# Optimization experiments

Measured on AMD Instinct MI355X. Metric: run time of the kernel, lower is better.

## Reference

```python
import jax, jax.numpy as jnp
import numpy as np

B, H, S, Dh = 4, 16, 2048, 64
NEG = -1.0e9


def setup_inputs() -> dict:
    key = jax.random.key(0)
    kq, kk, kv = jax.random.split(key, 3)
    q = jax.random.normal(kq, (B, H, S, Dh), dtype=jnp.float32)
    k = jax.random.normal(kk, (B, H, S, Dh), dtype=jnp.float32)
    v = jax.random.normal(kv, (B, H, S, Dh), dtype=jnp.float32)
    # causal mask: 1.0 where attention is disallowed (j > i), matching mask * -1e9
    mask = jnp.triu(jnp.ones((S, S), dtype=jnp.float32), k=1)[None, None, :, :]
    return {"q": q, "k": k, "v": v, "mask": mask}


def reference(q, k, v, mask):
    # scaled dot-product attention: softmax(QK^T / sqrt(Dh) + mask * -1e9) V
    dim_k = jnp.asarray(k.shape[-1], dtype=jnp.float32)
    logits = jnp.einsum("bhsd,bhtd->bhst", q, k) / jnp.sqrt(dim_k)
    logits = logits + mask * NEG
    weights = jax.nn.softmax(logits, axis=-1)
    return jnp.einsum("bhst,bhtd->bhsd", weights, v)
```

## Files before the change

kernel.cpp:

```cpp
#include <hip/hip_runtime.h>

#define S_LEN 2048
#define DH 64

typedef float f32x4 __attribute__((ext_vector_type(4)));
typedef __bf16 bf16x8 __attribute__((ext_vector_type(8)));

#define PTS 72
#define MFMA16(A, B, C) __builtin_amdgcn_mfma_f32_16x16x32_bf16(A, B, C, 0, 0, 0)

__device__ __forceinline__ unsigned short f2bf(float f) {
    unsigned u = __builtin_bit_cast(unsigned, f);
    u += 0x7fffu + ((u >> 16) & 1u);
    return (unsigned short)(u >> 16);
}

__device__ __forceinline__ uint4 pack8(const float* s) {
    unsigned short h[8];
#pragma unroll
    for (int i = 0; i < 8; ++i) h[i] = f2bf(s[i]);
    return *(const uint4*)h;
}

__device__ __forceinline__ unsigned pack_tr(float a, float b) {
    return __builtin_amdgcn_perm(__builtin_bit_cast(unsigned, b),
                                 __builtin_bit_cast(unsigned, a), 0x07060302u);
}

__device__ __forceinline__ bf16x8 ld128(const unsigned short* p) {
    return __builtin_bit_cast(bf16x8, *(const uint4*)p);
}

__device__ __forceinline__ bf16x8 ones8() {
    uint4 ou; ou.x = 0x3F803F80u; ou.y = ou.x; ou.z = ou.x; ou.w = ou.x;
    return __builtin_bit_cast(bf16x8, ou);
}

__global__ __launch_bounds__(256) void prep_kv(const float* __restrict__ k,
                                               const float* __restrict__ v,
                                               uint4* __restrict__ kimg,
                                               uint4* __restrict__ vimg) {
    __shared__ unsigned short tr[64 * 40];
    const int bid = blockIdx.x;
    const int t = threadIdx.x;
    if (bid < 4096) {
        const int r = t >> 3, b = t & 7;
        const int srcblk = b ^ (r & 7);
        const float* src = k + ((size_t)bid * 32 + r) * 64 + srcblk * 8;
        float buf[8];
        *(float4*)&buf[0] = *(const float4*)src;
        *(float4*)&buf[4] = *(const float4*)(src + 4);
        kimg[(size_t)bid * 256 + t] = pack8(buf);
    } else {
        const int vb = bid - 4096;
        const int r = t >> 3, cb = t & 7;
        const float* src = v + ((size_t)vb * 32 + r) * 64 + cb * 8;
        float buf[8];
        *(float4*)&buf[0] = *(const float4*)src;
        *(float4*)&buf[4] = *(const float4*)(src + 4);
#pragma unroll
        for (int i = 0; i < 8; ++i)
            tr[(cb * 8 + i) * 40 + r] = f2bf(buf[i]);
        __syncthreads();
        const int d = t >> 2, kb = t & 3;
        const int skb = kb ^ ((d >> 1) & 3);
        vimg[(size_t)vb * 256 + t] = *(const uint4*)&tr[d * 40 + skb * 8];
    }
}

template <int DIAG>
__device__ __forceinline__ void body64(
    const unsigned short* __restrict__ kt, const unsigned short* __restrict__ vt,
    unsigned short* __restrict__ pw0, unsigned short* __restrict__ pw1,
    const bf16x8* qf, f32x4 acc[2][4], f32x4* accl,
    int jt, int qbase, int quad, int c)
{
    const int sw = c & 7;
    const bf16x8 ones = ones8();
    const int MTN = (DIAG == 1) ? 2 : 4;

#pragma unroll
    for (int mt = 0; mt < MTN; ++mt) {
        const unsigned short* kr = kt + (mt * 16 + c) * 64;
        bf16x8 ka0 = ld128(kr + ((quad ^ sw) << 3));
        bf16x8 ka1 = ld128(kr + (((quad | 4) ^ sw) << 3));
        f32x4 s0 = (f32x4){0.f, 0.f, 0.f, 0.f};
        f32x4 s1 = (f32x4){0.f, 0.f, 0.f, 0.f};
        s0 = MFMA16(ka0, qf[0], s0);  s0 = MFMA16(ka1, qf[1], s0);
        s1 = MFMA16(ka0, qf[2], s1);  s1 = MFMA16(ka1, qf[3], s1);

        const bool MASKMT = (DIAG == 1) || (DIAG == 2 && mt >= 2);
#pragma unroll
        for (int s = 0; s < 2; ++s) {
            const f32x4 st = s ? s1 : s0;
            const int ig = qbase + s * 16 + c;
            float p[4];
#pragma unroll
            for (int r = 0; r < 4; ++r) {
                float e = __builtin_amdgcn_exp2f(st[r]);
                if (MASKMT) {
                    const int jg = jt * 64 + mt * 16 + quad * 4 + r;
                    e = (jg > ig) ? 0.f : e;
                }
                p[r] = e;
            }
            unsigned a = pack_tr(p[0], p[1]);
            unsigned b = pack_tr(p[2], p[3]);
            unsigned* pb = (unsigned*)(s ? pw1 : pw0) + c * (PTS / 2) + mt * 8 + quad * 2;
            *(uint2*)pb = make_uint2(a, b);
        }
    }

    bf16x8 pf00 = ld128(pw0 + c * PTS + quad * 8);
    bf16x8 pf10 = ld128(pw1 + c * PTS + quad * 8);
    accl[0] = MFMA16(pf00, ones, accl[0]);
    accl[1] = MFMA16(pf10, ones, accl[1]);
    bf16x8 pf01, pf11;
    if (DIAG != 1) {
        pf01 = ld128(pw0 + c * PTS + 32 + quad * 8);
        pf11 = ld128(pw1 + c * PTS + 32 + quad * 8);
        accl[0] = MFMA16(pf01, ones, accl[0]);
        accl[1] = MFMA16(pf11, ones, accl[1]);
    }

    const int vsw = (c >> 1) & 3;
#pragma unroll
    for (int dc = 0; dc < 4; ++dc) {
        const unsigned short* vr = vt + (dc * 16 + c) * 32 + ((quad ^ vsw) << 3);
        bf16x8 vf0 = ld128(vr);
        acc[0][dc] = MFMA16(pf00, vf0, acc[0][dc]);
        acc[1][dc] = MFMA16(pf10, vf0, acc[1][dc]);
        if (DIAG != 1) {
            bf16x8 vf1 = ld128(vr + 2048);
            acc[0][dc] = MFMA16(pf01, vf1, acc[0][dc]);
            acc[1][dc] = MFMA16(pf11, vf1, acc[1][dc]);
        }
    }
}

__global__ __launch_bounds__(256, 4) void fa_kernel(
    const float* __restrict__ q,
    const uint4* __restrict__ kimg,
    const uint4* __restrict__ vimg,
    float* __restrict__ out)
{
    __shared__ unsigned short kt[64 * 64];
    __shared__ unsigned short vt[2 * 64 * 32];
    __shared__ unsigned short pt[4][2][16 * PTS];

    const int tid  = threadIdx.x;
    const int lane = tid & 63;
    const int wave = tid >> 6;
    const int quad = lane >> 4;
    const int c    = lane & 15;

    const int bid = blockIdx.x;
    const int bh  = bid & 63;
    static const int qperm[16] = {15, 14, 13, 12, 8, 9, 10, 11,
                                  6, 5, 4, 3, 1, 2, 7, 0};
    const int qblk = qperm[bid >> 6];

    const int wt      = qblk * 4 + wave;
    const int qbase   = wt * 32;
    const int my_diag = wt >> 1;
    const int jt_last = 2 * qblk + 1;

    const size_t head_off = (size_t)bh * S_LEN * DH;

    const float SCALE = 0.125f * 1.4426950408889634f;
    bf16x8 qf[4];
#pragma unroll
    for (int s = 0; s < 2; ++s) {
        const float* qrow = q + head_off + (size_t)(qbase + s * 16 + c) * DH;
        float t0[8], t1[8];
#pragma unroll
        for (int i = 0; i < 8; ++i) t0[i] = qrow[quad * 8 + i] * SCALE;
#pragma unroll
        for (int i = 0; i < 8; ++i) t1[i] = qrow[32 + quad * 8 + i] * SCALE;
        qf[s * 2 + 0] = __builtin_bit_cast(bf16x8, pack8(t0));
        qf[s * 2 + 1] = __builtin_bit_cast(bf16x8, pack8(t1));
    }

    f32x4 acc[2][4];
#pragma unroll
    for (int s = 0; s < 2; ++s)
#pragma unroll
        for (int dc = 0; dc < 4; ++dc) acc[s][dc] = (f32x4){0.f, 0.f, 0.f, 0.f};
    f32x4 accl[2];
    accl[0] = (f32x4){0.f, 0.f, 0.f, 0.f};
    accl[1] = (f32x4){0.f, 0.f, 0.f, 0.f};

    const uint4* kin = kimg + (size_t)bh * 64 * 256 + tid;
    const uint4* vin = vimg + (size_t)bh * 64 * 256 + tid;
    unsigned short* pw0 = pt[wave][0];
    unsigned short* pw1 = pt[wave][1];

    uint4 kA = kin[0], kB = kin[256];
    uint4 vA = vin[0], vB = vin[256];
    for (int jt = 0; jt <= jt_last; ++jt) {
        __syncthreads();
        ((uint4*)kt)[tid] = kA;  ((uint4*)kt)[tid + 256] = kB;
        ((uint4*)vt)[tid] = vA;  ((uint4*)vt)[tid + 256] = vB;
        if (jt < jt_last) {
            kA = kin[(jt + 1) * 512];  kB = kin[(jt + 1) * 512 + 256];
            vA = vin[(jt + 1) * 512];  vB = vin[(jt + 1) * 512 + 256];
        }
        __syncthreads();

        if (jt < my_diag) {
            body64<0>(kt, vt, pw0, pw1, qf, acc, accl, jt, qbase, quad, c);
        } else if (jt == my_diag) {
            if ((wt & 1) == 0)
                body64<1>(kt, vt, pw0, pw1, qf, acc, accl, jt, qbase, quad, c);
            else
                body64<2>(kt, vt, pw0, pw1, qf, acc, accl, jt, qbase, quad, c);
        }
    }

    float* ob = out + head_off;
#pragma unroll
    for (int s = 0; s < 2; ++s) {
        float linv[4];
#pragma unroll
        for (int r = 0; r < 4; ++r) linv[r] = 1.0f / accl[s][r];
#pragma unroll
        for (int dc = 0; dc < 4; ++dc)
#pragma unroll
            for (int r = 0; r < 4; ++r) {
                const size_t idx =
                    (size_t)(qbase + s * 16 + quad * 4 + r) * DH + dc * 16 + c;
                ob[idx] = acc[s][dc][r] * linv[r];
            }
    }
}

#define KT_STRIDE 88
#define VT_STRIDE 36
__global__ __launch_bounds__(256) void fa_kernel_fb(
    const float* __restrict__ q, const float* __restrict__ k,
    const float* __restrict__ v, float* __restrict__ out)
{
    __shared__ unsigned short kts[32 * KT_STRIDE];
    __shared__ unsigned short vts[64 * VT_STRIDE];
    __shared__ unsigned short pts[4][16 * 40];
    const int tid = threadIdx.x, lane = tid & 63, wave = tid >> 6;
    const int quad = lane >> 4, c = lane & 15;
    const int bid = blockIdx.x, bh = bid & 63, qblk = 31 - (bid >> 6);
    const int qtile = qblk * 4 + wave, qbase = qtile * 16;
    const int my_diag = qtile >> 1, jt_last = (qblk * 4 + 3) >> 1;
    const size_t head_off = (size_t)bh * S_LEN * DH;
    const float* qrow = q + head_off + (size_t)(qbase + c) * DH;
    float qtmp[8];
#pragma unroll
    for (int i = 0; i < 8; ++i) qtmp[i] = qrow[quad * 8 + i];
    bf16x8 qf0 = __builtin_bit_cast(bf16x8, pack8(qtmp));
#pragma unroll
    for (int i = 0; i < 8; ++i) qtmp[i] = qrow[32 + quad * 8 + i];
    bf16x8 qf1 = __builtin_bit_cast(bf16x8, pack8(qtmp));
    f32x4 acc[4];
#pragma unroll
    for (int dc = 0; dc < 4; ++dc) acc[dc] = (f32x4){0.f, 0.f, 0.f, 0.f};
    float m_run = -1e30f, l_run = 0.f;
    const int ig = qbase + c;
    const int srow = tid >> 3, sdb = tid & 7;
    const int vcol = (((srow >> 3) ^ (sdb & 3)) << 3) | (srow & 7);
    const float LOG2E = 1.4426950408889634f;
    for (int jt = 0; jt <= jt_last; ++jt) {
        __syncthreads();
        {
            const size_t g = head_off + (size_t)(jt * 32 + srow) * DH + sdb * 8;
            float kbuf[8];
            *(float4*)&kbuf[0] = *(const float4*)(k + g);
            *(float4*)&kbuf[4] = *(const float4*)(k + g + 4);
            *(uint4*)&kts[srow * KT_STRIDE + sdb * 8] = pack8(kbuf);
            float vbuf[8];
            *(float4*)&vbuf[0] = *(const float4*)(v + g);
            *(float4*)&vbuf[4] = *(const float4*)(v + g + 4);
#pragma unroll
            for (int i = 0; i < 8; ++i)
                vts[(sdb * 8 + i) * VT_STRIDE + vcol] = f2bf(vbuf[i]);
        }
        __syncthreads();
        if (jt > my_diag) continue;
        f32x4 st[2];
#pragma unroll
        for (int mt = 0; mt < 2; ++mt) {
            const unsigned short* krow = &kts[(mt * 16 + c) * KT_STRIDE + quad * 8];
            bf16x8 ka0 = __builtin_bit_cast(bf16x8, *(const uint4*)krow);
            bf16x8 ka1 = __builtin_bit_cast(bf16x8, *(const uint4*)(krow + 32));
            f32x4 a = (f32x4){0.f, 0.f, 0.f, 0.f};
            a = MFMA16(ka0, qf0, a);
            a = MFMA16(ka1, qf1, a);
            st[mt] = a;
        }
        float tv[8];
#pragma unroll
        for (int mt = 0; mt < 2; ++mt)
#pragma unroll
            for (int r = 0; r < 4; ++r) {
                const int jg = jt * 32 + mt * 16 + quad * 4 + r;
                const float s = st[mt][r] * 0.125f;
                tv[mt * 4 + r] = (jg > ig) ? -1e30f : s;
            }
        float tm = tv[0];
#pragma unroll
        for (int i = 1; i < 8; ++i) tm = fmaxf(tm, tv[i]);
        tm = fmaxf(tm, __shfl_xor(tm, 16, 64));
        tm = fmaxf(tm, __shfl_xor(tm, 32, 64));
        const float m_new = fmaxf(m_run, tm);
        const float mb = m_new * LOG2E;
        float p[8], ps = 0.f;
#pragma unroll
        for (int i = 0; i < 8; ++i) {
            p[i] = __builtin_amdgcn_exp2f(tv[i] * LOG2E - mb);
            ps += p[i];
        }
        ps += __shfl_xor(ps, 16, 64);
        ps += __shfl_xor(ps, 32, 64);
        const float alpha = __builtin_amdgcn_exp2f((m_run - m_new) * LOG2E);
        l_run = l_run * alpha + ps;
        m_run = m_new;
        unsigned short* pwf = pts[wave];
#pragma unroll
        for (int mt = 0; mt < 2; ++mt)
#pragma unroll
            for (int r = 0; r < 4; ++r)
                pwf[c * 40 + mt * 16 + quad * 4 + r] = f2bf(p[mt * 4 + r]);
        float ar[4];
#pragma unroll
        for (int r = 0; r < 4; ++r)
            ar[r] = __shfl(alpha, (quad << 4) + quad * 4 + r, 64);
#pragma unroll
        for (int dc = 0; dc < 4; ++dc)
#pragma unroll
            for (int r = 0; r < 4; ++r) acc[dc][r] *= ar[r];
        bf16x8 pf = __builtin_bit_cast(bf16x8, *(const uint4*)&pwf[c * 40 + quad * 8]);
#pragma unroll
        for (int dc = 0; dc < 4; ++dc) {
            const int vrow = dc * 16 + c;
            const int blk = quad ^ ((vrow >> 3) & 3);
            const unsigned short* vp = &vts[vrow * VT_STRIDE + blk * 8];
            uint2 a0 = *(const uint2*)vp;
            uint2 a1 = *(const uint2*)(vp + 4);
            uint4 u; u.x = a0.x; u.y = a0.y; u.z = a1.x; u.w = a1.y;
            bf16x8 vf = __builtin_bit_cast(bf16x8, u);
            acc[dc] = MFMA16(pf, vf, acc[dc]);
        }
    }
    float linv[4];
#pragma unroll
    for (int r = 0; r < 4; ++r) {
        const float lr = __shfl(l_run, (quad << 4) + quad * 4 + r, 64);
        linv[r] = 1.0f / lr;
    }
    float* ob = out + head_off;
#pragma unroll
    for (int dc = 0; dc < 4; ++dc)
#pragma unroll
        for (int r = 0; r < 4; ++r) {
            const size_t idx = (size_t)(qbase + quad * 4 + r) * DH + dc * 16 + c;
            ob[idx] = acc[dc][r] * linv[r];
        }
}

extern "C" void kernel_launch(void* const* d_in, const int* in_sizes, int n_in,
                              void* d_out, int out_size, void* d_ws, size_t ws_size,
                              hipStream_t stream) {
    const float* q = (const float*)d_in[0];
    const float* k = (const float*)d_in[1];
    const float* v = (const float*)d_in[2];
    float* o = (float*)d_out;
    const size_t need = (size_t)2 * 64 * 64 * 4096;
    if (ws_size >= need) {
        uint4* kimg = (uint4*)d_ws;
        uint4* vimg = kimg + (size_t)64 * 64 * 256;
        hipLaunchKernelGGL(prep_kv, dim3(8192), dim3(256), 0, stream, k, v, kimg, vimg);
        hipLaunchKernelGGL(fa_kernel, dim3(1024), dim3(256), 0, stream, q, kimg, vimg, o);
    } else {
        hipLaunchKernelGGL(fa_kernel_fb, dim3(2048), dim3(256), 0, stream, q, k, v, o);
    }
}
```

Before: 185.2 us.

## Split attention blocks to 2 waves per 64-row query tile, 2048 blocks

Reworks the main attention kernel from 4-wave blocks covering 128 query rows to 2-wave blocks covering 64 query rows, launching 2048 blocks of 128 threads. Each block now loads only the K/V tiles up to its own diagonal, so waves no longer sit idle while their block-mates process extra tiles, and the causal triangle is split more finely. Blocks are launched in descending-work order instead of the old permutation. The cost is that each loaded K/V tile is shared by fewer waves (more global/LDS traffic per unit of work), each thread holds more prefetch registers, and barrier overhead per wave goes up.

```diff
diff --git a/kernel.cpp b/kernel.cpp
--- a/kernel.cpp
+++ b/kernel.cpp
@@ -138,7 +138,7 @@
     }
 }
 
-__global__ __launch_bounds__(256, 4) void fa_kernel(
+__global__ __launch_bounds__(128, 3) void fa_kernel(
     const float* __restrict__ q,
     const uint4* __restrict__ kimg,
     const uint4* __restrict__ vimg,
@@ -146,7 +146,7 @@
 {
     __shared__ unsigned short kt[64 * 64];
     __shared__ unsigned short vt[2 * 64 * 32];
-    __shared__ unsigned short pt[4][2][16 * PTS];
+    __shared__ unsigned short pt[2][2][16 * PTS];
 
     const int tid  = threadIdx.x;
     const int lane = tid & 63;
@@ -156,14 +156,10 @@
 
     const int bid = blockIdx.x;
     const int bh  = bid & 63;
-    static const int qperm[16] = {15, 14, 13, 12, 8, 9, 10, 11,
-                                  6, 5, 4, 3, 1, 2, 7, 0};
-    const int qblk = qperm[bid >> 6];
-
-    const int wt      = qblk * 4 + wave;
-    const int qbase   = wt * 32;
-    const int my_diag = wt >> 1;
-    const int jt_last = 2 * qblk + 1;
+    const int g   = 31 - (bid >> 6);
+
+    const int wt    = 2 * g + wave;
+    const int qbase = wt * 32;
 
     const size_t head_off = (size_t)bh * S_LEN * DH;
 
@@ -190,27 +186,39 @@
     accl[0] = (f32x4){0.f, 0.f, 0.f, 0.f};
     accl[1] = (f32x4){0.f, 0.f, 0.f, 0.f};
 
-    const uint4* kin = kimg + (size_t)bh * 64 * 256 + tid;
-    const uint4* vin = vimg + (size_t)bh * 64 * 256 + tid;
+    const uint4* kin = kimg + (size_t)bh * 64 * 256;
+    const uint4* vin = vimg + (size_t)bh * 64 * 256;
     unsigned short* pw0 = pt[wave][0];
     unsigned short* pw1 = pt[wave][1];
 
-    uint4 kA = kin[0], kB = kin[256];
-    uint4 vA = vin[0], vB = vin[256];
-    for (int jt = 0; jt <= jt_last; ++jt) {
-        __syncthreads();
-        ((uint4*)kt)[tid] = kA;  ((uint4*)kt)[tid + 256] = kB;
-        ((uint4*)vt)[tid] = vA;  ((uint4*)vt)[tid + 256] = vB;
-        if (jt < jt_last) {
-            kA = kin[(jt + 1) * 512];  kB = kin[(jt + 1) * 512 + 256];
-            vA = vin[(jt + 1) * 512];  vB = vin[(jt + 1) * 512 + 256];
-        }
-        __syncthreads();
-
-        if (jt < my_diag) {
+    uint4 kR[4], vR[4];
+#pragma unroll
+    for (int i = 0; i < 4; ++i) {
+        kR[i] = kin[tid + i * 128];
+        vR[i] = vin[tid + i * 128];
+    }
+
+    for (int jt = 0; jt <= g; ++jt) {
+        __syncthreads();
+#pragma unroll
+        for (int i = 0; i < 4; ++i) {
+            ((uint4*)kt)[tid + i * 128] = kR[i];
+            ((uint4*)vt)[tid + i * 128] = vR[i];
+        }
+        if (jt < g) {
+            const int base = (jt + 1) * 512 + tid;
+#pragma unroll
+            for (int i = 0; i < 4; ++i) {
+                kR[i] = kin[base + i * 128];
+                vR[i] = vin[base + i * 128];
+            }
+        }
+        __syncthreads();
+
+        if (jt < g) {
             body64<0>(kt, vt, pw0, pw1, qf, acc, accl, jt, qbase, quad, c);
-        } else if (jt == my_diag) {
-            if ((wt & 1) == 0)
+        } else {
+            if (wave == 0)
                 body64<1>(kt, vt, pw0, pw1, qf, acc, accl, jt, qbase, quad, c);
             else
                 body64<2>(kt, vt, pw0, pw1, qf, acc, accl, jt, qbase, quad, c);
@@ -268,14 +276,14 @@
     for (int jt = 0; jt <= jt_last; ++jt) {
         __syncthreads();
         {
-            const size_t g = head_off + (size_t)(jt * 32 + srow) * DH + sdb * 8;
+            const size_t gaddr = head_off + (size_t)(jt * 32 + srow) * DH + sdb * 8;
             float kbuf[8];
-            *(float4*)&kbuf[0] = *(const float4*)(k + g);
-            *(float4*)&kbuf[4] = *(const float4*)(k + g + 4);
+            *(float4*)&kbuf[0] = *(const float4*)(k + gaddr);
+            *(float4*)&kbuf[4] = *(const float4*)(k + gaddr + 4);
             *(uint4*)&kts[srow * KT_STRIDE + sdb * 8] = pack8(kbuf);
             float vbuf[8];
-            *(float4*)&vbuf[0] = *(const float4*)(v + g);
-            *(float4*)&vbuf[4] = *(const float4*)(v + g + 4);
+            *(float4*)&vbuf[0] = *(const float4*)(v + gaddr);
+            *(float4*)&vbuf[4] = *(const float4*)(v + gaddr + 4);
 #pragma unroll
             for (int i = 0; i < 8; ++i)
                 vts[(sdb * 8 + i) * VT_STRIDE + vcol] = f2bf(vbuf[i]);
@@ -375,7 +383,7 @@
         uint4* kimg = (uint4*)d_ws;
         uint4* vimg = kimg + (size_t)64 * 64 * 256;
         hipLaunchKernelGGL(prep_kv, dim3(8192), dim3(256), 0, stream, k, v, kimg, vimg);
-        hipLaunchKernelGGL(fa_kernel, dim3(1024), dim3(256), 0, stream, q, kimg, vimg, o);
+        hipLaunchKernelGGL(fa_kernel, dim3(2048), dim3(128), 0, stream, q, kimg, vimg, o);
     } else {
         hipLaunchKernelGGL(fa_kernel_fb, dim3(2048), dim3(256), 0, stream, q, k, v, o);
     }
```

Result: slower. 319.5 us (+72.5%).

## Pair causal query blocks per workgroup to balance triangular work

Applied to the files above, without the earlier changes.

Each workgroup now handles two query blocks in sequence, pr and 15-pr, so every workgroup does about the same number of key tiles under the causal mask. The grid shrinks from 1024 to 512 workgroups and the qperm static scheduling table goes away. This removes tail imbalance between short and long causal rows, but leaves fewer workgroups to hide latency, and the K/V stream restarts for the second block. A variable rename in the fallback kernel is cosmetic.

```diff
diff --git a/kernel.cpp b/kernel.cpp
--- a/kernel.cpp
+++ b/kernel.cpp
@@ -156,81 +156,83 @@
 
     const int bid = blockIdx.x;
     const int bh  = bid & 63;
-    static const int qperm[16] = {15, 14, 13, 12, 8, 9, 10, 11,
-                                  6, 5, 4, 3, 1, 2, 7, 0};
-    const int qblk = qperm[bid >> 6];
-
-    const int wt      = qblk * 4 + wave;
-    const int qbase   = wt * 32;
-    const int my_diag = wt >> 1;
-    const int jt_last = 2 * qblk + 1;
+    const int pr  = bid >> 6;
 
     const size_t head_off = (size_t)bh * S_LEN * DH;
-
-    const float SCALE = 0.125f * 1.4426950408889634f;
-    bf16x8 qf[4];
-#pragma unroll
-    for (int s = 0; s < 2; ++s) {
-        const float* qrow = q + head_off + (size_t)(qbase + s * 16 + c) * DH;
-        float t0[8], t1[8];
-#pragma unroll
-        for (int i = 0; i < 8; ++i) t0[i] = qrow[quad * 8 + i] * SCALE;
-#pragma unroll
-        for (int i = 0; i < 8; ++i) t1[i] = qrow[32 + quad * 8 + i] * SCALE;
-        qf[s * 2 + 0] = __builtin_bit_cast(bf16x8, pack8(t0));
-        qf[s * 2 + 1] = __builtin_bit_cast(bf16x8, pack8(t1));
-    }
-
-    f32x4 acc[2][4];
-#pragma unroll
-    for (int s = 0; s < 2; ++s)
-#pragma unroll
-        for (int dc = 0; dc < 4; ++dc) acc[s][dc] = (f32x4){0.f, 0.f, 0.f, 0.f};
-    f32x4 accl[2];
-    accl[0] = (f32x4){0.f, 0.f, 0.f, 0.f};
-    accl[1] = (f32x4){0.f, 0.f, 0.f, 0.f};
-
-    const uint4* kin = kimg + (size_t)bh * 64 * 256 + tid;
-    const uint4* vin = vimg + (size_t)bh * 64 * 256 + tid;
+    const uint4* kin = kimg + (size_t)bh * 64 * 256;
+    const uint4* vin = vimg + (size_t)bh * 64 * 256;
     unsigned short* pw0 = pt[wave][0];
     unsigned short* pw1 = pt[wave][1];
-
-    uint4 kA = kin[0], kB = kin[256];
-    uint4 vA = vin[0], vB = vin[256];
-    for (int jt = 0; jt <= jt_last; ++jt) {
-        __syncthreads();
-        ((uint4*)kt)[tid] = kA;  ((uint4*)kt)[tid + 256] = kB;
-        ((uint4*)vt)[tid] = vA;  ((uint4*)vt)[tid + 256] = vB;
-        if (jt < jt_last) {
-            kA = kin[(jt + 1) * 512];  kB = kin[(jt + 1) * 512 + 256];
-            vA = vin[(jt + 1) * 512];  vB = vin[(jt + 1) * 512 + 256];
-        }
-        __syncthreads();
-
-        if (jt < my_diag) {
-            body64<0>(kt, vt, pw0, pw1, qf, acc, accl, jt, qbase, quad, c);
-        } else if (jt == my_diag) {
-            if ((wt & 1) == 0)
-                body64<1>(kt, vt, pw0, pw1, qf, acc, accl, jt, qbase, quad, c);
-            else
-                body64<2>(kt, vt, pw0, pw1, qf, acc, accl, jt, qbase, quad, c);
-        }
-    }
-
+    const float SCALE = 0.125f * 1.4426950408889634f;
     float* ob = out + head_off;
-#pragma unroll
-    for (int s = 0; s < 2; ++s) {
-        float linv[4];
-#pragma unroll
-        for (int r = 0; r < 4; ++r) linv[r] = 1.0f / accl[s][r];
-#pragma unroll
-        for (int dc = 0; dc < 4; ++dc)
-#pragma unroll
-            for (int r = 0; r < 4; ++r) {
-                const size_t idx =
-                    (size_t)(qbase + s * 16 + quad * 4 + r) * DH + dc * 16 + c;
-                ob[idx] = acc[s][dc][r] * linv[r];
+
+#pragma unroll 1
+    for (int ph = 0; ph < 2; ++ph) {
+        const int qblk = ph ? (15 - pr) : pr;
+        const int wt      = qblk * 4 + wave;
+        const int qbase   = wt * 32;
+        const int my_diag = wt >> 1;
+        const int jt_last = 2 * qblk + 1;
+
+        bf16x8 qf[4];
+#pragma unroll
+        for (int s = 0; s < 2; ++s) {
+            const float* qrow = q + head_off + (size_t)(qbase + s * 16 + c) * DH;
+            float t0[8], t1[8];
+#pragma unroll
+            for (int i = 0; i < 8; ++i) t0[i] = qrow[quad * 8 + i] * SCALE;
+#pragma unroll
+            for (int i = 0; i < 8; ++i) t1[i] = qrow[32 + quad * 8 + i] * SCALE;
+            qf[s * 2 + 0] = __builtin_bit_cast(bf16x8, pack8(t0));
+            qf[s * 2 + 1] = __builtin_bit_cast(bf16x8, pack8(t1));
+        }
+
+        f32x4 acc[2][4];
+#pragma unroll
+        for (int s = 0; s < 2; ++s)
+#pragma unroll
+            for (int dc = 0; dc < 4; ++dc) acc[s][dc] = (f32x4){0.f, 0.f, 0.f, 0.f};
+        f32x4 accl[2];
+        accl[0] = (f32x4){0.f, 0.f, 0.f, 0.f};
+        accl[1] = (f32x4){0.f, 0.f, 0.f, 0.f};
+
+        uint4 kA = kin[tid], kB = kin[tid + 256];
+        uint4 vA = vin[tid], vB = vin[tid + 256];
+        for (int jt = 0; jt <= jt_last; ++jt) {
+            __syncthreads();
+            ((uint4*)kt)[tid] = kA;  ((uint4*)kt)[tid + 256] = kB;
+            ((uint4*)vt)[tid] = vA;  ((uint4*)vt)[tid + 256] = vB;
+            if (jt < jt_last) {
+                const int base = (jt + 1) * 512 + tid;
+                kA = kin[base];  kB = kin[base + 256];
+                vA = vin[base];  vB = vin[base + 256];
             }
+            __syncthreads();
+
+            if (jt < my_diag) {
+                body64<0>(kt, vt, pw0, pw1, qf, acc, accl, jt, qbase, quad, c);
+            } else if (jt == my_diag) {
+                if ((wt & 1) == 0)
+                    body64<1>(kt, vt, pw0, pw1, qf, acc, accl, jt, qbase, quad, c);
+                else
+                    body64<2>(kt, vt, pw0, pw1, qf, acc, accl, jt, qbase, quad, c);
+            }
+        }
+
+#pragma unroll
+        for (int s = 0; s < 2; ++s) {
+            float linv[4];
+#pragma unroll
+            for (int r = 0; r < 4; ++r) linv[r] = 1.0f / accl[s][r];
+#pragma unroll
+            for (int dc = 0; dc < 4; ++dc)
+#pragma unroll
+                for (int r = 0; r < 4; ++r) {
+                    const size_t idx =
+                        (size_t)(qbase + s * 16 + quad * 4 + r) * DH + dc * 16 + c;
+                    ob[idx] = acc[s][dc][r] * linv[r];
+                }
+        }
     }
 }
 
@@ -268,14 +270,14 @@
     for (int jt = 0; jt <= jt_last; ++jt) {
         __syncthreads();
         {
-            const size_t g = head_off + (size_t)(jt * 32 + srow) * DH + sdb * 8;
+            const size_t gaddr = head_off + (size_t)(jt * 32 + srow) * DH + sdb * 8;
             float kbuf[8];
-            *(float4*)&kbuf[0] = *(const float4*)(k + g);
-            *(float4*)&kbuf[4] = *(const float4*)(k + g + 4);
+            *(float4*)&kbuf[0] = *(const float4*)(k + gaddr);
+            *(float4*)&kbuf[4] = *(const float4*)(k + gaddr + 4);
             *(uint4*)&kts[srow * KT_STRIDE + sdb * 8] = pack8(kbuf);
             float vbuf[8];
-            *(float4*)&vbuf[0] = *(const float4*)(v + g);
-            *(float4*)&vbuf[4] = *(const float4*)(v + g + 4);
+            *(float4*)&vbuf[0] = *(const float4*)(v + gaddr);
+            *(float4*)&vbuf[4] = *(const float4*)(v + gaddr + 4);
 #pragma unroll
             for (int i = 0; i < 8; ++i)
                 vts[(sdb * 8 + i) * VT_STRIDE + vcol] = f2bf(vbuf[i]);
@@ -375,7 +377,7 @@
         uint4* kimg = (uint4*)d_ws;
         uint4* vimg = kimg + (size_t)64 * 64 * 256;
         hipLaunchKernelGGL(prep_kv, dim3(8192), dim3(256), 0, stream, k, v, kimg, vimg);
-        hipLaunchKernelGGL(fa_kernel, dim3(1024), dim3(256), 0, stream, q, kimg, vimg, o);
+        hipLaunchKernelGGL(fa_kernel, dim3(512), dim3(256), 0, stream, q, kimg, vimg, o);
     } else {
         hipLaunchKernelGGL(fa_kernel_fb, dim3(2048), dim3(256), 0, stream, q, k, v, o);
     }
```

After: 192.9 us. 1.04x slower.
